# Kernel optimization log

Hardware: AMD Instinct MI355X
Metric: run time of the kernel (lower is better)

The kernel has to match this reference:

```python
import jax, jax.numpy as jnp
import numpy as np
import math
from jax import lax

B, NP1, M, D, H, L, DFF = 16, 65, 256, 512, 8, 3, 2048
EPS_PROJ = 0.01  # MartingaleProjectionLayer is built with epsilon=0.01
LN_EPS = 1e-5


def _pos_encoding(n, d):
    pos = np.arange(n, dtype=np.float32)[:, None]
    div = np.exp(np.arange(0, d, 2, dtype=np.float32) * (-math.log(10000.0) / d))
    pe = np.zeros((n, d), dtype=np.float32)
    pe[:, 0::2] = np.sin(pos * div)
    pe[:, 1::2] = np.cos(pos * div)
    return jnp.asarray(pe)


def setup_inputs() -> dict:
    key = jax.random.key(0)
    ks = jax.random.split(key, 32)
    s = 0.02
    marg = jax.random.uniform(ks[0], (B, NP1, M), jnp.float32)
    marg = marg / marg.sum(axis=-1, keepdims=True)  # proper distributions
    return {
        "marginals": marg,
        "x_grid": jnp.linspace(-3.0, 3.0, M, dtype=jnp.float32),
        "conv_w": jax.random.normal(ks[1], (128, 1, 5), jnp.float32) * s,
        "conv_b": jax.random.normal(ks[2], (128,), jnp.float32) * s,
        "fc_w": jax.random.normal(ks[3], (128, D), jnp.float32) * s,
        "fc_b": jax.random.normal(ks[4], (D,), jnp.float32) * s,
        "ln0_g": jnp.ones((D,), jnp.float32),
        "ln0_b": jnp.zeros((D,), jnp.float32),
        "pos_enc": _pos_encoding(NP1, D),
        "qkv_w": jax.random.normal(ks[5], (L, 3 * D, D), jnp.float32) * s,
        "qkv_b": jax.random.normal(ks[6], (L, 3 * D), jnp.float32) * s,
        "out_w": jax.random.normal(ks[7], (L, D, D), jnp.float32) * s,
        "out_b": jax.random.normal(ks[8], (L, D), jnp.float32) * s,
        "ln1_g": jnp.ones((L, D), jnp.float32),
        "ln1_b": jnp.zeros((L, D), jnp.float32),
        "ff1_w": jax.random.normal(ks[9], (L, DFF, D), jnp.float32) * s,
        "ff1_b": jax.random.normal(ks[10], (L, DFF), jnp.float32) * s,
        "ff2_w": jax.random.normal(ks[11], (L, D, DFF), jnp.float32) * s,
        "ff2_b": jax.random.normal(ks[12], (L, D), jnp.float32) * s,
        "ln2_g": jnp.ones((L, D), jnp.float32),
        "ln2_b": jnp.zeros((L, D), jnp.float32),
        "u_w": jax.random.normal(ks[13], (M, D), jnp.float32) * s,
        "u_b": jax.random.normal(ks[14], (M,), jnp.float32) * s,
        "h_w": jax.random.normal(ks[15], (M, D), jnp.float32) * s,
        "h_b": jax.random.normal(ks[16], (M,), jnp.float32) * s,
    }


def _ln(x, g, b):
    mu = x.mean(axis=-1, keepdims=True)
    var = ((x - mu) ** 2).mean(axis=-1, keepdims=True)
    return (x - mu) * lax.rsqrt(var + LN_EPS) * g + b


def _gelu(x):
    return jax.nn.gelu(x, approximate=False)  # torch default exact GELU


def reference(marginals, x_grid, conv_w, conv_b, fc_w, fc_b, ln0_g, ln0_b,
              pos_enc, qkv_w, qkv_b, out_w, out_b, ln1_g, ln1_b,
              ff1_w, ff1_b, ff2_w, ff2_b, ln2_g, ln2_b, u_w, u_b, h_w, h_b):
    b, np1, m = marginals.shape
    n = np1 - 1
    d = fc_w.shape[1]
    nh = H
    dh = d // nh

    # ---- marginal embedding: Conv1d(1,128,k=5,pad=2) -> mean over grid -> FC+LN+GELU
    x = marginals.reshape(b * np1, 1, m)
    y = lax.conv_general_dilated(x, conv_w, (1,), [(2, 2)],
                                 dimension_numbers=("NCH", "OIH", "NCH"))
    y = y + conv_b[None, :, None]          # (b*np1, 128, m)
    emb = y.mean(axis=2)                   # (b*np1, 128)
    emb = _gelu(_ln(emb @ fc_w + fc_b, ln0_g, ln0_b))
    xs = emb.reshape(b, np1, d) + pos_enc[None, :np1, :]

    # ---- post-norm transformer encoder (dropout off / eval mode)
    scale = 1.0 / math.sqrt(dh)
    for l in range(L):
        qkv = xs @ qkv_w[l].T + qkv_b[l]                        # (b, s, 3d)
        q, k, v = jnp.split(qkv, 3, axis=-1)
        q = q.reshape(b, np1, nh, dh).transpose(0, 2, 1, 3)
        k = k.reshape(b, np1, nh, dh).transpose(0, 2, 1, 3)
        v = v.reshape(b, np1, nh, dh).transpose(0, 2, 1, 3)
        att = jax.nn.softmax(jnp.einsum("bhqd,bhkd->bhqk", q, k) * scale, axis=-1)
        o = jnp.einsum("bhqk,bhkd->bhqd", att, v)
        o = o.transpose(0, 2, 1, 3).reshape(b, np1, d)
        o = o @ out_w[l].T + out_b[l]
        xs = _ln(xs + o, ln1_g[l], ln1_b[l])
        ff = _gelu(xs @ ff1_w[l].T + ff1_b[l]) @ ff2_w[l].T + ff2_b[l]
        xs = _ln(xs + ff, ln2_g[l], ln2_b[l])

    u_pot = xs @ u_w.T + u_b                                    # (b, np1, M)
    h_raw = xs[:, :n, :] @ h_w.T + h_b                          # (b, n, M)

    # ---- vectorized martingale projection over all N timesteps
    x_diff = x_grid[:, None] - x_grid[None, :]                  # (M, M)
    h_kernel = h_raw[..., None] * x_diff                        # (b, n, M, M)
    P = jax.nn.softmax(h_kernel / EPS_PROJ, axis=-1)
    expected_next = jnp.einsum("bnij,j->bni", P, x_grid)
    drift = expected_next - x_grid                              # (b, n, M)
    mu = marginals[:, :n, :]
    weight_drift = (mu * drift).sum(axis=-1, keepdims=True)
    correction = weight_drift / (mu.sum(axis=-1, keepdims=True) + 1e-8)
    h_pot = h_raw - correction
    return (u_pot, h_pot)
```

## Files before the change

kernel.cpp:

```cpp
#include <hip/hip_runtime.h>
#include <math.h>


#define BT   1040
#define NP1  65
#define Dm   512
#define MG   256

typedef short short8 __attribute__((ext_vector_type(8)));
typedef float f32x4  __attribute__((ext_vector_type(4)));
typedef unsigned short u16;

__device__ __forceinline__ u16 f2bf(float f) {
  unsigned int u = __float_as_uint(f);
  u += 0x7FFF + ((u >> 16) & 1);
  return (u16)(u >> 16);
}

__device__ __forceinline__ float gelu_exact(float x) {
  return 0.5f * x * (1.0f + erff(x * 0.70710678118654752f));
}

__device__ __forceinline__ void async16(const u16* g, u16* l) {
  __builtin_amdgcn_global_load_lds(
      (const __attribute__((address_space(1))) unsigned int*)g,
      (__attribute__((address_space(3))) unsigned int*)l, 16, 0, 0);
}

__device__ __forceinline__ float wred(float v) {
#pragma unroll
  for (int o = 32; o; o >>= 1) v += __shfl_xor(v, o, 64);
  return v;
}

__device__ __forceinline__ float block_reduce_sum(float v, float* s) {
#pragma unroll
  for (int off = 32; off; off >>= 1) v += __shfl_down(v, off, 64);
  int lane = threadIdx.x & 63, wid = threadIdx.x >> 6;
  __syncthreads();
  if (lane == 0) s[wid] = v;
  __syncthreads();
  return s[0] + s[1] + s[2] + s[3];
}

__device__ __forceinline__ float f_closed(float a) {
  const float tf = 2.3529411765f;
  float t = a * tf;
  float s = fabsf(t);
  float E;
  if (s < 1e-4f) {
    E = 127.5f - 5461.25f * t;
  } else {
    float u = s * 256.0f;
    float term2 = (u < 80.0f) ? 256.0f / expm1f(u) : 0.0f;
    float Epos = 1.0f / expm1f(s) - term2;
    E = (t > 0.0f) ? Epos : 255.0f - Epos;
  }
  return -3.0f + 0.0235294118f * E;
}

__global__ __launch_bounds__(256) void prep_kernel(
    const float* __restrict__ qkv_w, const float* __restrict__ out_w,
    const float* __restrict__ ff1_w, const float* __restrict__ ff2_w,
    const float* __restrict__ u_w,   const float* __restrict__ h_w,
    u16* __restrict__ wdst,
    const float* __restrict__ marg, const float* __restrict__ conv_w,
    const float* __restrict__ conv_b, const float* __restrict__ fc_w,
    const float* __restrict__ fc_b, const float* __restrict__ g,
    const float* __restrict__ bb, const float* __restrict__ pos,
    float* __restrict__ xs, u16* __restrict__ xsb)
{
  const int tid = threadIdx.x;
  if (blockIdx.x < 512) {
    const size_t O1 = 2359296, O2 = 3145728, O3 = 6291456;
    const size_t O4 = 9437184, O5 = 9568256, TOT4 = 9699328 / 4;
    for (size_t e4 = (size_t)blockIdx.x * 256 + tid; e4 < TOT4;
         e4 += (size_t)512 * 256) {
      size_t e = e4 * 4;
      const float* src;
      if      (e < O1) src = qkv_w + e;
      else if (e < O2) src = out_w + (e - O1);
      else if (e < O3) src = ff1_w + (e - O2);
      else if (e < O4) src = ff2_w + (e - O3);
      else if (e < O5) src = u_w   + (e - O4);
      else             src = h_w   + (e - O5);
      float4 v = *(const float4*)src;
      unsigned int lo = (unsigned int)f2bf(v.x) | ((unsigned int)f2bf(v.y) << 16);
      unsigned int hi = (unsigned int)f2bf(v.z) | ((unsigned int)f2bf(v.w) << 16);
      *(uint2*)(wdst + e) = make_uint2(lo, hi);
    }
    return;
  }
  __shared__ float es[4][128];
  __shared__ float sS[4];
  __shared__ float edge[4][4];
  __shared__ float red[4];
  const int t0 = (blockIdx.x - 512) * 4;
  const int lane = tid & 63, wave = tid >> 6;
  {
    float4 mv = *(const float4*)(marg + (size_t)(t0 + wave) * MG + lane * 4);
    float S = wred(mv.x + mv.y + mv.z + mv.w);
    if (lane == 0) sS[wave] = S;
  }
  if (tid < 16) {
    int k = tid >> 2, e = tid & 3;
    int idx = (e < 2) ? e : (e + 252);
    edge[k][e] = marg[(size_t)(t0 + k) * MG + idx];
  }
  __syncthreads();
  if (tid < 128) {
    int o = tid;
    float w0 = conv_w[o*5+0], w1 = conv_w[o*5+1], w2 = conv_w[o*5+2];
    float w3 = conv_w[o*5+3], w4 = conv_w[o*5+4], cb = conv_b[o];
#pragma unroll
    for (int k = 0; k < 4; ++k) {
      float S = sS[k];
      float x0 = edge[k][0], x1 = edge[k][1], x254 = edge[k][2], x255 = edge[k][3];
      es[k][o] = (w0*(S - x254 - x255) + w1*(S - x255) + w2*S
                + w3*(S - x0) + w4*(S - x0 - x1)) * (1.0f/256.0f) + cb;
    }
  }
  __syncthreads();
  float b0 = fc_b[tid], b1 = fc_b[tid + 256];
  float z[4][2];
#pragma unroll
  for (int k = 0; k < 4; ++k) { z[k][0] = b0; z[k][1] = b1; }
#pragma unroll 4
  for (int o = 0; o < 128; ++o) {
    float f0 = fc_w[(size_t)o*Dm + tid];
    float f1 = fc_w[(size_t)o*Dm + tid + 256];
#pragma unroll
    for (int k = 0; k < 4; ++k) {
      float e = es[k][o];
      z[k][0] += e * f0; z[k][1] += e * f1;
    }
  }
  float g0 = g[tid], g1 = g[tid+256], e0 = bb[tid], e1 = bb[tid+256];
#pragma unroll
  for (int k = 0; k < 4; ++k) {
    float mu = block_reduce_sum(z[k][0] + z[k][1], red) * (1.0f/512.0f);
    float d0 = z[k][0] - mu, d1 = z[k][1] - mu;
    float var = block_reduce_sum(d0*d0 + d1*d1, red) * (1.0f/512.0f);
    float inv = rsqrtf(var + 1e-5f);
    int t = t0 + k, p = t % NP1;
    float y0 = gelu_exact(d0*inv*g0 + e0) + pos[(size_t)p*Dm + tid];
    float y1 = gelu_exact(d1*inv*g1 + e1) + pos[(size_t)p*Dm + tid + 256];
    xs[(size_t)t*Dm + tid]        = y0;
    xs[(size_t)t*Dm + tid + 256]  = y1;
    xsb[(size_t)t*Dm + tid]       = f2bf(y0);
    xsb[(size_t)t*Dm + tid + 256] = f2bf(y1);
  }
}

template<int SPLITS, int MODE>
__global__ __launch_bounds__(256) void gemm_mfma(
    const u16* __restrict__ A, const u16* __restrict__ Bw,
    const float* __restrict__ bias, float* __restrict__ Cf,
    u16* __restrict__ Cb, float* __restrict__ C2,
    const float* __restrict__ bias2, int Mrows, int N, int K)
{
  __shared__ u16 Asl[2][8*64*8];
  __shared__ u16 Bsl[2][8*64*8];
  const int tid = threadIdx.x;
  const int row0 = blockIdx.y * 64, col0 = blockIdx.x * 64;
  const int Ks = K / SPLITS, kbase = (int)blockIdx.z * Ks;
  const int lane = tid & 63, wave = tid >> 6;
  const int wm = (wave >> 1) * 32, wn = (wave & 1) * 32;
  const int l15 = lane & 15, q = lane >> 4;

  f32x4 acc[2][2];
  acc[0][0] = (f32x4){0,0,0,0}; acc[0][1] = (f32x4){0,0,0,0};
  acc[1][0] = (f32x4){0,0,0,0}; acc[1][1] = (f32x4){0,0,0,0};

  const int arow = min(row0 + lane, Mrows - 1);
  const size_t abase = (size_t)arow * K;
  const size_t bbase = (size_t)(col0 + lane) * K;
  const int c0w = wave * 2;

#pragma unroll
  for (int i = 0; i < 2; ++i) {
    int c = c0w + i;
    async16(A + abase + kbase + c * 8, &Asl[0][(size_t)(c * 64 + lane) * 8]);
    async16(Bw + bbase + kbase + c * 8, &Bsl[0][(size_t)(c * 64 + lane) * 8]);
  }

  const int nk = Ks >> 6;
  for (int t = 0; t < nk; ++t) {
    const int cur = t & 1;
    if (t + 1 < nk) {
      const int nxt = cur ^ 1;
      const int kk = kbase + (t + 1) * 64;
#pragma unroll
      for (int i = 0; i < 2; ++i) {
        int c = c0w + i;
        async16(A + abase + kk + c * 8, &Asl[nxt][(size_t)(c * 64 + lane) * 8]);
        async16(Bw + bbase + kk + c * 8, &Bsl[nxt][(size_t)(c * 64 + lane) * 8]);
      }
      asm volatile("s_waitcnt vmcnt(4)" ::: "memory");
    } else {
      asm volatile("s_waitcnt vmcnt(0)" ::: "memory");
    }
    __builtin_amdgcn_s_barrier();
#pragma unroll
    for (int tt = 0; tt < 2; ++tt) {
      int cc = tt * 4 + q;
      short8 af[2], bf[2];
#pragma unroll
      for (int mi = 0; mi < 2; ++mi)
        af[mi] = *(short8*)&Asl[cur][(size_t)(cc*64 + wm + mi*16 + l15) * 8];
#pragma unroll
      for (int ni = 0; ni < 2; ++ni)
        bf[ni] = *(short8*)&Bsl[cur][(size_t)(cc*64 + wn + ni*16 + l15) * 8];
#pragma unroll
      for (int mi = 0; mi < 2; ++mi)
#pragma unroll
        for (int ni = 0; ni < 2; ++ni)
          acc[mi][ni] = __builtin_amdgcn_mfma_f32_16x16x32_bf16(
              af[mi], bf[ni], acc[mi][ni], 0, 0, 0);
    }
    __builtin_amdgcn_s_barrier();
  }

  float* Cp = Cf;
  if (MODE == 2) Cp += (size_t)blockIdx.z * (size_t)Mrows * N;
#pragma unroll
  for (int mi = 0; mi < 2; ++mi) {
#pragma unroll
    for (int ni = 0; ni < 2; ++ni) {
      int col = col0 + wn + ni*16 + l15;
#pragma unroll
      for (int r = 0; r < 4; ++r) {
        int row = row0 + wm + mi*16 + q*4 + r;
        if (row < Mrows) {
          float v = acc[mi][ni][r];
          if (MODE == 0) {
            Cp[(size_t)row*N + col] = v + bias[col];
          } else if (MODE == 1) {
            Cb[(size_t)row*N + col] = f2bf(gelu_exact(v + bias[col]));
          } else if (MODE == 2) {
            Cp[(size_t)row*N + col] = v;
          } else {
            if (col < 256) Cf[(size_t)row*256 + col]         = v + bias[col];
            else           C2[(size_t)row*256 + (col - 256)] = v + bias2[col - 256];
          }
        }
      }
    }
  }
}

template<int S>
__global__ __launch_bounds__(256) void add_ln4(
    float* __restrict__ xs, u16* __restrict__ xsb,
    const float* __restrict__ part, const float* __restrict__ bias,
    const float* __restrict__ g, const float* __restrict__ bb)
{
  const int lane = threadIdx.x & 63, wave = threadIdx.x >> 6;
  const int t = blockIdx.x * 4 + wave;
  const int c0 = lane * 8;
  float* xp = xs + (size_t)t * Dm;
  float v[8];
  {
    float4 a0 = *(const float4*)(xp + c0), a1 = *(const float4*)(xp + c0 + 4);
    float4 b0 = *(const float4*)(bias + c0), b1 = *(const float4*)(bias + c0 + 4);
    v[0]=a0.x+b0.x; v[1]=a0.y+b0.y; v[2]=a0.z+b0.z; v[3]=a0.w+b0.w;
    v[4]=a1.x+b1.x; v[5]=a1.y+b1.y; v[6]=a1.z+b1.z; v[7]=a1.w+b1.w;
  }
#pragma unroll
  for (int s = 0; s < S; ++s) {
    const float* pp = part + (size_t)s*BT*Dm + (size_t)t*Dm + c0;
    float4 q0 = *(const float4*)pp, q1 = *(const float4*)(pp + 4);
    v[0]+=q0.x; v[1]+=q0.y; v[2]+=q0.z; v[3]+=q0.w;
    v[4]+=q1.x; v[5]+=q1.y; v[6]+=q1.z; v[7]+=q1.w;
  }
  float s1 = 0.f;
#pragma unroll
  for (int j = 0; j < 8; ++j) s1 += v[j];
  float mu = wred(s1) * (1.0f/512.0f);
  float s2 = 0.f;
#pragma unroll
  for (int j = 0; j < 8; ++j) { float d = v[j]-mu; s2 += d*d; }
  float inv = rsqrtf(wred(s2) * (1.0f/512.0f) + 1e-5f);
  float4 g0 = *(const float4*)(g + c0), g1 = *(const float4*)(g + c0 + 4);
  float4 e0 = *(const float4*)(bb + c0), e1 = *(const float4*)(bb + c0 + 4);
  float gg[8] = {g0.x,g0.y,g0.z,g0.w,g1.x,g1.y,g1.z,g1.w};
  float ee[8] = {e0.x,e0.y,e0.z,e0.w,e1.x,e1.y,e1.z,e1.w};
  float y[8]; u16 yb[8];
#pragma unroll
  for (int j = 0; j < 8; ++j) { y[j] = (v[j]-mu)*inv*gg[j] + ee[j]; yb[j] = f2bf(y[j]); }
  *(float4*)(xp + c0)     = make_float4(y[0],y[1],y[2],y[3]);
  *(float4*)(xp + c0 + 4) = make_float4(y[4],y[5],y[6],y[7]);
  *(short8*)(xsb + (size_t)t*Dm + c0) = *(short8*)yb;
}

__global__ __launch_bounds__(256) void attn_kernel(
    const float* __restrict__ qkv, u16* __restrict__ obufb)
{
  __shared__ float qv[65][67];
  __shared__ float ks[65][67];
  __shared__ float ss[65][67];
  const int b = blockIdx.x >> 3, h = blockIdx.x & 7;
  const int tid = threadIdx.x;
  const float* base = qkv + (size_t)b * NP1 * 1536 + h * 64;
  for (int idx = tid; idx < NP1 * 16; idx += 256) {
    int t = idx >> 4, c = (idx & 15) << 2;
    const float* p = base + (size_t)t * 1536 + c;
    float4 q4 = *(const float4*)(p);
    float4 k4 = *(const float4*)(p + 512);
    qv[t][c] = q4.x; qv[t][c+1] = q4.y; qv[t][c+2] = q4.z; qv[t][c+3] = q4.w;
    ks[t][c] = k4.x; ks[t][c+1] = k4.y; ks[t][c+2] = k4.z; ks[t][c+3] = k4.w;
  }
  __syncthreads();
#pragma unroll
  for (int it = 0; it < 2; ++it) {
    int tile = it * 256 + tid;
    if (tile < 289) {
      int ti = (tile / 17) * 4, tj = (tile % 17) * 4;
      const float* qr[4]; const float* kr[4];
#pragma unroll
      for (int i = 0; i < 4; ++i) { qr[i] = qv[min(ti + i, 64)]; kr[i] = ks[min(tj + i, 64)]; }
      float acc[4][4] = {};
      for (int d = 0; d < 64; ++d) {
        float a[4], bvv[4];
#pragma unroll
        for (int i = 0; i < 4; ++i) { a[i] = qr[i][d]; bvv[i] = kr[i][d]; }
#pragma unroll
        for (int i = 0; i < 4; ++i)
#pragma unroll
          for (int j = 0; j < 4; ++j) acc[i][j] += a[i] * bvv[j];
      }
#pragma unroll
      for (int i = 0; i < 4; ++i)
        if (ti + i < 65)
#pragma unroll
          for (int j = 0; j < 4; ++j)
            if (tj + j < 65) ss[ti + i][tj + j] = acc[i][j] * 0.125f;
    }
  }
  __syncthreads();
  for (int idx = tid; idx < NP1 * 16; idx += 256) {
    int t = idx >> 4, c = (idx & 15) << 2;
    float4 v4 = *(const float4*)(base + (size_t)t * 1536 + 1024 + c);
    qv[t][c] = v4.x; qv[t][c+1] = v4.y; qv[t][c+2] = v4.z; qv[t][c+3] = v4.w;
  }
  if (tid < 65) {
    float mx = -1e30f;
    for (int j = 0; j < 65; ++j) mx = fmaxf(mx, ss[tid][j]);
    float s = 0.0f;
    for (int j = 0; j < 65; ++j) { float e = expf(ss[tid][j] - mx); ss[tid][j] = e; s += e; }
    float inv = 1.0f / s;
    for (int j = 0; j < 65; ++j) ss[tid][j] *= inv;
  }
  __syncthreads();
#pragma unroll
  for (int it = 0; it < 2; ++it) {
    int tile = it * 256 + tid;
    if (tile < 272) {
      int ti = (tile >> 4) * 4, d0 = (tile & 15) * 4;
      const float* sr[4];
#pragma unroll
      for (int i = 0; i < 4; ++i) sr[i] = ss[min(ti + i, 64)];
      float acc[4][4] = {};
      for (int j = 0; j < 65; ++j) {
        float v0 = qv[j][d0], v1 = qv[j][d0+1], v2 = qv[j][d0+2], v3 = qv[j][d0+3];
#pragma unroll
        for (int i = 0; i < 4; ++i) {
          float s = sr[i][j];
          acc[i][0] += s * v0; acc[i][1] += s * v1;
          acc[i][2] += s * v2; acc[i][3] += s * v3;
        }
      }
#pragma unroll
      for (int i = 0; i < 4; ++i)
        if (ti + i < 65) {
          ushort4 o;
          o.x = f2bf(acc[i][0]); o.y = f2bf(acc[i][1]);
          o.z = f2bf(acc[i][2]); o.w = f2bf(acc[i][3]);
          *(ushort4*)(obufb + (size_t)(b * NP1 + ti + i) * Dm + h * 64 + d0) = o;
        }
    }
  }
}

__global__ __launch_bounds__(256) void proj_closed(
    const float* __restrict__ hbuf, const float* __restrict__ marg,
    const float* __restrict__ xg, float* __restrict__ out_h)
{
  const int tid = threadIdx.x, lane = tid & 63, wave = tid >> 6;
  const int rr = blockIdx.x * 4 + wave;
  const int b = rr >> 6, n = rr & 63;
  const int row = b * NP1 + n;
  const int i0 = lane * 4;
  float4 a4 = *(const float4*)(hbuf + (size_t)row * MG + i0);
  float4 x4 = *(const float4*)(xg + i0);
  float4 m4 = *(const float4*)(marg + (size_t)row * MG + i0);
  float av[4] = {a4.x, a4.y, a4.z, a4.w};
  float xv[4] = {x4.x, x4.y, x4.z, x4.w};
  float uv[4] = {m4.x, m4.y, m4.z, m4.w};
  float wd = 0.f, ms = 0.f;
#pragma unroll
  for (int k = 0; k < 4; ++k) {
    float drift = f_closed(av[k]) - xv[k];
    wd += uv[k] * drift; ms += uv[k];
  }
  wd = wred(wd); ms = wred(ms);
  float corr = wd / (ms + 1e-8f);
  *(float4*)(out_h + ((size_t)(b * 64 + n)) * MG + i0) =
      make_float4(av[0]-corr, av[1]-corr, av[2]-corr, av[3]-corr);
}

extern "C" void kernel_launch(void* const* d_in, const int* in_sizes, int n_in,
                              void* d_out, int out_size, void* d_ws, size_t ws_size,
                              hipStream_t stream)
{
  const float* marg   = (const float*)d_in[0];
  const float* xg     = (const float*)d_in[1];
  const float* conv_w = (const float*)d_in[2];
  const float* conv_b = (const float*)d_in[3];
  const float* fc_w   = (const float*)d_in[4];
  const float* fc_b   = (const float*)d_in[5];
  const float* ln0_g  = (const float*)d_in[6];
  const float* ln0_b  = (const float*)d_in[7];
  const float* pos    = (const float*)d_in[8];
  const float* qkv_w  = (const float*)d_in[9];
  const float* qkv_b  = (const float*)d_in[10];
  const float* out_w  = (const float*)d_in[11];
  const float* out_b  = (const float*)d_in[12];
  const float* ln1_g  = (const float*)d_in[13];
  const float* ln1_b  = (const float*)d_in[14];
  const float* ff1_w  = (const float*)d_in[15];
  const float* ff1_b  = (const float*)d_in[16];
  const float* ff2_w  = (const float*)d_in[17];
  const float* ff2_b  = (const float*)d_in[18];
  const float* ln2_g  = (const float*)d_in[19];
  const float* ln2_b  = (const float*)d_in[20];
  const float* u_w    = (const float*)d_in[21];
  const float* u_b    = (const float*)d_in[22];
  const float* h_w    = (const float*)d_in[23];
  const float* h_b    = (const float*)d_in[24];
  float* out = (float*)d_out;

  float* ws = (float*)d_ws;
  float* xs      = ws;
  float* qkvbuf  = ws + 532480;
  float* part    = ws + 2129920;
  float* hbuf    = ws + 4259840;
  u16*   xsb     = (u16*)(ws + 4526080);
  u16*   obufb   = (u16*)(ws + 4792320);
  u16*   ffb     = (u16*)(ws + 5058560);
  u16*   wbf     = (u16*)(ws + 6123520);

  const u16* qkv_bw = wbf;
  const u16* out_bw = wbf + 2359296;
  const u16* ff1_bw = wbf + 3145728;
  const u16* ff2_bw = wbf + 6291456;
  const u16* uh_bw  = wbf + 9437184;

  prep_kernel<<<772, 256, 0, stream>>>(
      qkv_w, out_w, ff1_w, ff2_w, u_w, h_w, wbf,
      marg, conv_w, conv_b, fc_w, fc_b, ln0_g, ln0_b, pos, xs, xsb);

  for (int l = 0; l < 3; ++l) {
    gemm_mfma<1,0><<<dim3(24, 17), 256, 0, stream>>>(
        xsb, qkv_bw + (size_t)l*786432, qkv_b + l*1536, qkvbuf,
        nullptr, nullptr, nullptr, BT, 1536, 512);
    attn_kernel<<<128, 256, 0, stream>>>(qkvbuf, obufb);
    gemm_mfma<2,2><<<dim3(8, 17, 2), 256, 0, stream>>>(
        obufb, out_bw + (size_t)l*262144, nullptr, part,
        nullptr, nullptr, nullptr, BT, 512, 512);
    add_ln4<2><<<260, 256, 0, stream>>>(xs, xsb, part, out_b + l*512,
                                        ln1_g + l*512, ln1_b + l*512);
    gemm_mfma<1,1><<<dim3(32, 17), 256, 0, stream>>>(
        xsb, ff1_bw + (size_t)l*1048576, ff1_b + l*2048, nullptr,
        ffb, nullptr, nullptr, BT, 2048, 512);
    gemm_mfma<4,2><<<dim3(8, 17, 4), 256, 0, stream>>>(
        ffb, ff2_bw + (size_t)l*1048576, nullptr, part,
        nullptr, nullptr, nullptr, BT, 512, 2048);
    add_ln4<4><<<260, 256, 0, stream>>>(xs, xsb, part, ff2_b + l*512,
                                        ln2_g + l*512, ln2_b + l*512);
  }

  gemm_mfma<1,3><<<dim3(8, 17), 256, 0, stream>>>(
      xsb, uh_bw, u_b, out, nullptr, hbuf, h_b, BT, 512, 512);
  proj_closed<<<256, 256, 0, stream>>>(hbuf, marg, xg, out + 1040*256);
}
```

Baseline: 405.4 us.

## Fuse out-proj/FF2 GEMMs with residual LayerNorm and head GEMM with projection

Replaces the split-K GEMMs plus separate add+LayerNorm kernels with a row-block kernel. Each block computes 16 full rows of 512 output columns and applies bias, residual and LayerNorm in registers. The final u/h head GEMM is fused the same way with the martingale correction. This removes the partial-sum buffers and several launches per layer. In exchange, only 65 blocks run on a large GPU, and every block streams the whole weight matrix from global/L2 with only register-level prefetch, so occupancy and latency hiding get worse.

New measurement: 570.8 us. 1.41x slower.

```diff
diff --git a/kernel.cpp b/kernel.cpp
--- a/kernel.cpp
+++ b/kernel.cpp
@@ -152,18 +152,16 @@
   }
 }
 
-template<int SPLITS, int MODE>
+template<int MODE>
 __global__ __launch_bounds__(256) void gemm_mfma(
     const u16* __restrict__ A, const u16* __restrict__ Bw,
     const float* __restrict__ bias, float* __restrict__ Cf,
-    u16* __restrict__ Cb, float* __restrict__ C2,
-    const float* __restrict__ bias2, int Mrows, int N, int K)
+    u16* __restrict__ Cb, int Mrows, int N, int K)
 {
   __shared__ u16 Asl[2][8*64*8];
   __shared__ u16 Bsl[2][8*64*8];
   const int tid = threadIdx.x;
   const int row0 = blockIdx.y * 64, col0 = blockIdx.x * 64;
-  const int Ks = K / SPLITS, kbase = (int)blockIdx.z * Ks;
   const int lane = tid & 63, wave = tid >> 6;
   const int wm = (wave >> 1) * 32, wn = (wave & 1) * 32;
   const int l15 = lane & 15, q = lane >> 4;
@@ -180,21 +178,21 @@
 #pragma unroll
   for (int i = 0; i < 2; ++i) {
     int c = c0w + i;
-    async16(A + abase + kbase + c * 8, &Asl[0][(size_t)(c * 64 + lane) * 8]);
-    async16(Bw + bbase + kbase + c * 8, &Bsl[0][(size_t)(c * 64 + lane) * 8]);
-  }
-
-  const int nk = Ks >> 6;
+    async16(A + abase + c * 8, &Asl[0][(size_t)(c * 64 + lane) * 8]);
+    async16(Bw + bbase + c * 8, &Bsl[0][(size_t)(c * 64 + lane) * 8]);
+  }
+
+  const int nk = K >> 6;
   for (int t = 0; t < nk; ++t) {
     const int cur = t & 1;
     if (t + 1 < nk) {
       const int nxt = cur ^ 1;
-      const int kk = kbase + (t + 1) * 64;
+      const int kk = (t + 1) * 64;
 #pragma unroll
       for (int i = 0; i < 2; ++i) {
         int c = c0w + i;
-        async16(A + abase + kk + c * 8, &Asl[nxt][(size_t)(c * 64 + lane) * 8]);
-        async16(Bw + bbase + kk + c * 8, &Bsl[nxt][(size_t)(c * 64 + lane) * 8]);
+        async16(A + abase + kk + c * 8, &Asl[nxt][(size_t)(c*64 + lane)*8]);
+        async16(Bw + bbase + kk + c * 8, &Bsl[nxt][(size_t)(c*64 + lane)*8]);
       }
       asm volatile("s_waitcnt vmcnt(4)" ::: "memory");
     } else {
@@ -221,8 +219,6 @@
     __builtin_amdgcn_s_barrier();
   }
 
-  float* Cp = Cf;
-  if (MODE == 2) Cp += (size_t)blockIdx.z * (size_t)Mrows * N;
 #pragma unroll
   for (int mi = 0; mi < 2; ++mi) {
 #pragma unroll
@@ -234,14 +230,9 @@
         if (row < Mrows) {
           float v = acc[mi][ni][r];
           if (MODE == 0) {
-            Cp[(size_t)row*N + col] = v + bias[col];
-          } else if (MODE == 1) {
+            Cf[(size_t)row*N + col] = v + bias[col];
+          } else {
             Cb[(size_t)row*N + col] = f2bf(gelu_exact(v + bias[col]));
-          } else if (MODE == 2) {
-            Cp[(size_t)row*N + col] = v;
-          } else {
-            if (col < 256) Cf[(size_t)row*256 + col]         = v + bias[col];
-            else           C2[(size_t)row*256 + (col - 256)] = v + bias2[col - 256];
           }
         }
       }
@@ -249,48 +240,193 @@
   }
 }
 
-template<int S>
-__global__ __launch_bounds__(256) void add_ln4(
+template<int KK, int EPI>
+__global__ __launch_bounds__(256) void fused_row(
+    const u16* __restrict__ A, const u16* __restrict__ Bw,
+    const float* __restrict__ bias,
     float* __restrict__ xs, u16* __restrict__ xsb,
-    const float* __restrict__ part, const float* __restrict__ bias,
-    const float* __restrict__ g, const float* __restrict__ bb)
+    const float* __restrict__ g, const float* __restrict__ bb,
+    const float* __restrict__ bias2,
+    const float* __restrict__ marg, const float* __restrict__ xg,
+    float* __restrict__ outu, float* __restrict__ outh)
 {
-  const int lane = threadIdx.x & 63, wave = threadIdx.x >> 6;
-  const int t = blockIdx.x * 4 + wave;
-  const int c0 = lane * 8;
-  float* xp = xs + (size_t)t * Dm;
-  float v[8];
-  {
-    float4 a0 = *(const float4*)(xp + c0), a1 = *(const float4*)(xp + c0 + 4);
-    float4 b0 = *(const float4*)(bias + c0), b1 = *(const float4*)(bias + c0 + 4);
-    v[0]=a0.x+b0.x; v[1]=a0.y+b0.y; v[2]=a0.z+b0.z; v[3]=a0.w+b0.w;
-    v[4]=a1.x+b1.x; v[5]=a1.y+b1.y; v[6]=a1.z+b1.z; v[7]=a1.w+b1.w;
-  }
-#pragma unroll
-  for (int s = 0; s < S; ++s) {
-    const float* pp = part + (size_t)s*BT*Dm + (size_t)t*Dm + c0;
-    float4 q0 = *(const float4*)pp, q1 = *(const float4*)(pp + 4);
-    v[0]+=q0.x; v[1]+=q0.y; v[2]+=q0.z; v[3]+=q0.w;
-    v[4]+=q1.x; v[5]+=q1.y; v[6]+=q1.z; v[7]+=q1.w;
-  }
-  float s1 = 0.f;
-#pragma unroll
-  for (int j = 0; j < 8; ++j) s1 += v[j];
-  float mu = wred(s1) * (1.0f/512.0f);
-  float s2 = 0.f;
-#pragma unroll
-  for (int j = 0; j < 8; ++j) { float d = v[j]-mu; s2 += d*d; }
-  float inv = rsqrtf(wred(s2) * (1.0f/512.0f) + 1e-5f);
-  float4 g0 = *(const float4*)(g + c0), g1 = *(const float4*)(g + c0 + 4);
-  float4 e0 = *(const float4*)(bb + c0), e1 = *(const float4*)(bb + c0 + 4);
-  float gg[8] = {g0.x,g0.y,g0.z,g0.w,g1.x,g1.y,g1.z,g1.w};
-  float ee[8] = {e0.x,e0.y,e0.z,e0.w,e1.x,e1.y,e1.z,e1.w};
-  float y[8]; u16 yb[8];
-#pragma unroll
-  for (int j = 0; j < 8; ++j) { y[j] = (v[j]-mu)*inv*gg[j] + ee[j]; yb[j] = f2bf(y[j]); }
-  *(float4*)(xp + c0)     = make_float4(y[0],y[1],y[2],y[3]);
-  *(float4*)(xp + c0 + 4) = make_float4(y[4],y[5],y[6],y[7]);
-  *(short8*)(xsb + (size_t)t*Dm + c0) = *(short8*)yb;
+  constexpr int KC  = (KK < 1024) ? KK : 1024;
+  constexpr int NCH = KK / KC;
+  __shared__ u16 Alds[16 * KC];
+  __shared__ float red[4][16];
+  __shared__ float red2[4][16];
+  const int tid = threadIdx.x, lane = tid & 63, wave = tid >> 6;
+  const int l15 = lane & 15, q = lane >> 4;
+  const int r0 = blockIdx.x * 16;
+  const int gc0 = wave * 128;
+
+  f32x4 acc[8];
+#pragma unroll
+  for (int i = 0; i < 8; ++i) acc[i] = (f32x4){0,0,0,0};
+
+  for (int ch = 0; ch < NCH; ++ch) {
+    const int kc = ch * KC;
+    __syncthreads();
+    for (int idx = tid; idx < 2 * KC; idx += 256) {
+      int r = idx & 15, c = idx >> 4;
+      async16(A + (size_t)(r0 + r) * KK + kc + c * 8, &Alds[(size_t)idx * 8]);
+    }
+    asm volatile("s_waitcnt vmcnt(0)" ::: "memory");
+    __syncthreads();
+
+    constexpr int S = KC / 32;
+    short8 bcur[8], bnxt[8];
+#pragma unroll
+    for (int i = 0; i < 8; ++i)
+      bcur[i] = *(const short8*)&Bw[(size_t)(gc0 + i*16 + l15) * KK + kc + q * 8];
+    for (int s = 0; s < S; ++s) {
+      if (s + 1 < S) {
+#pragma unroll
+        for (int i = 0; i < 8; ++i)
+          bnxt[i] = *(const short8*)&Bw[(size_t)(gc0 + i*16 + l15) * KK
+                                        + kc + ((s + 1) * 4 + q) * 8];
+      }
+      short8 af = *(const short8*)&Alds[(size_t)((s * 4 + q) * 16 + l15) * 8];
+#pragma unroll
+      for (int i = 0; i < 8; ++i)
+        acc[i] = __builtin_amdgcn_mfma_f32_16x16x32_bf16(af, bcur[i], acc[i], 0, 0, 0);
+#pragma unroll
+      for (int i = 0; i < 8; ++i) bcur[i] = bnxt[i];
+    }
+  }
+
+  if (EPI == 0) {
+    float vv[8][4];
+#pragma unroll
+    for (int i = 0; i < 8; ++i) {
+      int col = gc0 + i*16 + l15;
+      float bcol = bias[col];
+#pragma unroll
+      for (int r = 0; r < 4; ++r) {
+        int gr = r0 + q*4 + r;
+        vv[i][r] = acc[i][r] + bcol + xs[(size_t)gr * Dm + col];
+      }
+    }
+    float ps[4];
+#pragma unroll
+    for (int r = 0; r < 4; ++r) {
+      float s = 0.f;
+#pragma unroll
+      for (int i = 0; i < 8; ++i) s += vv[i][r];
+      ps[r] = s;
+    }
+#pragma unroll
+    for (int o = 1; o < 16; o <<= 1)
+#pragma unroll
+      for (int r = 0; r < 4; ++r) ps[r] += __shfl_xor(ps[r], o, 64);
+    if (l15 == 0)
+#pragma unroll
+      for (int r = 0; r < 4; ++r) red[wave][q*4 + r] = ps[r];
+    __syncthreads();
+    float mu[4];
+#pragma unroll
+    for (int r = 0; r < 4; ++r) {
+      int rr = q*4 + r;
+      mu[r] = (red[0][rr] + red[1][rr] + red[2][rr] + red[3][rr]) * (1.0f/512.0f);
+    }
+    float ps2[4];
+#pragma unroll
+    for (int r = 0; r < 4; ++r) {
+      float s = 0.f;
+#pragma unroll
+      for (int i = 0; i < 8; ++i) { float d = vv[i][r] - mu[r]; s += d * d; }
+      ps2[r] = s;
+    }
+#pragma unroll
+    for (int o = 1; o < 16; o <<= 1)
+#pragma unroll
+      for (int r = 0; r < 4; ++r) ps2[r] += __shfl_xor(ps2[r], o, 64);
+    if (l15 == 0)
+#pragma unroll
+      for (int r = 0; r < 4; ++r) red2[wave][q*4 + r] = ps2[r];
+    __syncthreads();
+    float inv[4];
+#pragma unroll
+    for (int r = 0; r < 4; ++r) {
+      int rr = q*4 + r;
+      inv[r] = rsqrtf((red2[0][rr] + red2[1][rr] + red2[2][rr] + red2[3][rr])
+                      * (1.0f/512.0f) + 1e-5f);
+    }
+#pragma unroll
+    for (int i = 0; i < 8; ++i) {
+      int col = gc0 + i*16 + l15;
+      float gc = g[col], bc = bb[col];
+#pragma unroll
+      for (int r = 0; r < 4; ++r) {
+        int gr = r0 + q*4 + r;
+        float y = (vv[i][r] - mu[r]) * inv[r] * gc + bc;
+        xs[(size_t)gr * Dm + col] = y;
+        xsb[(size_t)gr * Dm + col] = f2bf(y);
+      }
+    }
+  } else {
+    float va[8][4];
+    if (wave >= 2) {
+      float wd[4] = {0.f,0.f,0.f,0.f}, ms[4] = {0.f,0.f,0.f,0.f};
+#pragma unroll
+      for (int i = 0; i < 8; ++i) {
+        int hcol = (gc0 - 256) + i*16 + l15;
+        float bcol = bias2[hcol];
+        float xv = xg[hcol];
+#pragma unroll
+        for (int r = 0; r < 4; ++r) {
+          int gr = r0 + q*4 + r;
+          float a = acc[i][r] + bcol;
+          va[i][r] = a;
+          float uvm = marg[(size_t)gr * MG + hcol];
+          wd[r] += uvm * (f_closed(a) - xv);
+          ms[r] += uvm;
+        }
+      }
+#pragma unroll
+      for (int o = 1; o < 16; o <<= 1)
+#pragma unroll
+        for (int r = 0; r < 4; ++r) {
+          wd[r] += __shfl_xor(wd[r], o, 64);
+          ms[r] += __shfl_xor(ms[r], o, 64);
+        }
+      if (l15 == 0)
+#pragma unroll
+        for (int r = 0; r < 4; ++r) {
+          red[wave][q*4 + r]  = wd[r];
+          red2[wave][q*4 + r] = ms[r];
+        }
+    }
+    __syncthreads();
+    if (wave < 2) {
+#pragma unroll
+      for (int i = 0; i < 8; ++i) {
+        int col = gc0 + i*16 + l15;
+        float bcol = bias[col];
+#pragma unroll
+        for (int r = 0; r < 4; ++r) {
+          int gr = r0 + q*4 + r;
+          outu[(size_t)gr * MG + col] = acc[i][r] + bcol;
+        }
+      }
+    } else {
+#pragma unroll
+      for (int i = 0; i < 8; ++i) {
+        int hcol = (gc0 - 256) + i*16 + l15;
+#pragma unroll
+        for (int r = 0; r < 4; ++r) {
+          int rr = q*4 + r;
+          int gr = r0 + rr;
+          int b = gr / NP1, n = gr - b * NP1;
+          if (n < 64) {
+            float corr = (red[2][rr] + red[3][rr])
+                       / (red2[2][rr] + red2[3][rr] + 1e-8f);
+            outh[(size_t)(b * 64 + n) * MG + hcol] = va[i][r] - corr;
+          }
+        }
+      }
+    }
+  }
 }
 
 __global__ __launch_bounds__(256) void attn_kernel(
@@ -380,33 +516,6 @@
         }
     }
   }
-}
-
-__global__ __launch_bounds__(256) void proj_closed(
-    const float* __restrict__ hbuf, const float* __restrict__ marg,
-    const float* __restrict__ xg, float* __restrict__ out_h)
-{
-  const int tid = threadIdx.x, lane = tid & 63, wave = tid >> 6;
-  const int rr = blockIdx.x * 4 + wave;
-  const int b = rr >> 6, n = rr & 63;
-  const int row = b * NP1 + n;
-  const int i0 = lane * 4;
-  float4 a4 = *(const float4*)(hbuf + (size_t)row * MG + i0);
-  float4 x4 = *(const float4*)(xg + i0);
-  float4 m4 = *(const float4*)(marg + (size_t)row * MG + i0);
-  float av[4] = {a4.x, a4.y, a4.z, a4.w};
-  float xv[4] = {x4.x, x4.y, x4.z, x4.w};
-  float uv[4] = {m4.x, m4.y, m4.z, m4.w};
-  float wd = 0.f, ms = 0.f;
-#pragma unroll
-  for (int k = 0; k < 4; ++k) {
-    float drift = f_closed(av[k]) - xv[k];
-    wd += uv[k] * drift; ms += uv[k];
-  }
-  wd = wred(wd); ms = wred(ms);
-  float corr = wd / (ms + 1e-8f);
-  *(float4*)(out_h + ((size_t)(b * 64 + n)) * MG + i0) =
-      make_float4(av[0]-corr, av[1]-corr, av[2]-corr, av[3]-corr);
 }
 
 extern "C" void kernel_launch(void* const* d_in, const int* in_sizes, int n_in,
@@ -443,8 +552,6 @@
   float* ws = (float*)d_ws;
   float* xs      = ws;
   float* qkvbuf  = ws + 532480;
-  float* part    = ws + 2129920;
-  float* hbuf    = ws + 4259840;
   u16*   xsb     = (u16*)(ws + 4526080);
   u16*   obufb   = (u16*)(ws + 4792320);
   u16*   ffb     = (u16*)(ws + 5058560);
@@ -461,26 +568,25 @@
       marg, conv_w, conv_b, fc_w, fc_b, ln0_g, ln0_b, pos, xs, xsb);
 
   for (int l = 0; l < 3; ++l) {
-    gemm_mfma<1,0><<<dim3(24, 17), 256, 0, stream>>>(
+    gemm_mfma<0><<<dim3(24, 17), 256, 0, stream>>>(
         xsb, qkv_bw + (size_t)l*786432, qkv_b + l*1536, qkvbuf,
-        nullptr, nullptr, nullptr, BT, 1536, 512);
+        nullptr, BT, 1536, 512);
     attn_kernel<<<128, 256, 0, stream>>>(qkvbuf, obufb);
-    gemm_mfma<2,2><<<dim3(8, 17, 2), 256, 0, stream>>>(
-        obufb, out_bw + (size_t)l*262144, nullptr, part,
-        nullptr, nullptr, nullptr, BT, 512, 512);
-    add_ln4<2><<<260, 256, 0, stream>>>(xs, xsb, part, out_b + l*512,
-                                        ln1_g + l*512, ln1_b + l*512);
-    gemm_mfma<1,1><<<dim3(32, 17), 256, 0, stream>>>(
+    fused_row<512, 0><<<65, 256, 0, stream>>>(
+        obufb, out_bw + (size_t)l*262144, out_b + l*512,
+        xs, xsb, ln1_g + l*512, ln1_b + l*512,
+        nullptr, nullptr, nullptr, nullptr, nullptr);
+    gemm_mfma<1><<<dim3(32, 17), 256, 0, stream>>>(
         xsb, ff1_bw + (size_t)l*1048576, ff1_b + l*2048, nullptr,
-        ffb, nullptr, nullptr, BT, 2048, 512);
-    gemm_mfma<4,2><<<dim3(8, 17, 4), 256, 0, stream>>>(
-        ffb, ff2_bw + (size_t)l*1048576, nullptr, part,
-        nullptr, nullptr, nullptr, BT, 512, 2048);
-    add_ln4<4><<<260, 256, 0, stream>>>(xs, xsb, part, ff2_b + l*512,
-                                        ln2_g + l*512, ln2_b + l*512);
-  }
-
-  gemm_mfma<1,3><<<dim3(8, 17), 256, 0, stream>>>(
-      xsb, uh_bw, u_b, out, nullptr, hbuf, h_b, BT, 512, 512);
-  proj_closed<<<256, 256, 0, stream>>>(hbuf, marg, xg, out + 1040*256);
-}
+        ffb, BT, 2048, 512);
+    fused_row<2048, 0><<<65, 256, 0, stream>>>(
+        ffb, ff2_bw + (size_t)l*1048576, ff2_b + l*512,
+        xs, xsb, ln2_g + l*512, ln2_b + l*512,
+        nullptr, nullptr, nullptr, nullptr, nullptr);
+  }
+
+  fused_row<512, 1><<<65, 256, 0, stream>>>(
+      xsb, uh_bw, u_b,
+      nullptr, nullptr, nullptr, nullptr,
+      h_b, marg, xg, out, out + 1040*256);
+}
```
